# Kernel tuning notes

Hardware: AMD Instinct MI355X
Metric: run time of the kernel (lower is better)

Reference implementation:

```python
import jax, jax.numpy as jnp
import numpy as np

CDIM = 32
SCALES = (1, 16, 64, 256, 1024, 4096)  # last entry == T
INV_TEMP = 100.0
ENT_W = 0.1
COMMIT_W = 0.2
Q_SCALE = 1.0 / float(np.sqrt(CDIM))


def _interp_area(x, pt):
    # x: [B, T, C] -> [B, pt, C]; T divisible by pt so 'area' == block mean
    B, T, C = x.shape
    return x.reshape(B, pt, T // pt, C).mean(axis=2)


def _interp_linear(x, T):
    # x: [B, pt, C] -> [B, T, C]; mode='linear', align_corners=False
    pt = x.shape[1]
    pos = (jnp.arange(T, dtype=jnp.float32) + 0.5) * (pt / T) - 0.5
    pos = jnp.clip(pos, 0.0, pt - 1.0)
    lo = jnp.floor(pos).astype(jnp.int32)
    hi = jnp.minimum(lo + 1, pt - 1)
    w = (pos - lo.astype(jnp.float32))[None, :, None]
    return x[:, lo] * (1.0 - w) + x[:, hi] * w


def _bsq(f):
    # L2 normalize (torch F.normalize: clamp_min on norm)
    f = f / jnp.maximum(jnp.linalg.norm(f, axis=-1, keepdims=True), 1e-12)
    # sign quantize with STE
    zhat = jnp.where(f > 0, Q_SCALE, -Q_SCALE).astype(f.dtype)
    quantized = f + jax.lax.stop_gradient(zhat - f)
    # soft entropy loss
    p = jax.nn.sigmoid(-4.0 * f * (INV_TEMP / float(np.sqrt(CDIM))))
    prob = jnp.stack([p, 1.0 - p], axis=-1)  # [B, T, C, 2]
    ent = lambda c: -(c * jnp.log(c + 1e-8)).sum(axis=-1)
    per_sample_entropy = ent(prob).sum(axis=-1).mean()
    avg_prob = prob.mean(axis=(0, 1))  # [C, 2]
    cb_entropy = ent(avg_prob).sum()
    entropy_penalty = (per_sample_entropy - cb_entropy) / INV_TEMP
    commit = ((jax.lax.stop_gradient(quantized) - f) ** 2).sum(axis=-1).mean()
    aux = entropy_penalty * ENT_W + commit * COMMIT_W
    bits = (quantized > 0).astype(jnp.int32)
    return quantized, bits, aux


def setup_inputs() -> dict:
    key = jax.random.key(0)
    B, T, C = 128, SCALES[-1], CDIM
    return {"f_BTC": jax.random.normal(key, (B, T, C), dtype=jnp.float32)}


def reference(f_BTC):
    B, T, C = f_BTC.shape
    quantized_out = jnp.zeros_like(f_BTC)
    residual = f_BTC
    losses, bit_list = [], []
    for pt in SCALES:
        interp_res = _interp_area(residual, pt) if pt != T else residual
        q, bits, loss = _bsq(interp_res)
        q = _interp_linear(q, T) if pt != T else q
        residual = residual - jax.lax.stop_gradient(q)
        quantized_out = quantized_out + q
        bit_list.append(bits)
        losses.append(loss)
    all_losses = jnp.stack(losses, axis=-1)       # [num_scales]
    all_bits = jnp.concatenate(bit_list, axis=1)  # [B, sum(SCALES), C]
    return quantized_out, all_bits, all_losses
```

## Files before the change

kernel.cpp:

```cpp
#include <hip/hip_runtime.h>
#include <hip/hip_bf16.h>
#include <cstddef>
#include <cstdint>

#define NB 128
#define NT 4096
#define NC 32
#define BITROWS 5457
#define QV_ROWS 1361
#define QOUT_ELEMS (NB*NT*NC)
#define BITS_ELEMS (NB*BITROWS*NC)

#define ACC_OFF  22298624
#define S16_OFF  22302720

__device__ __constant__ float kQSC = 0.17677669529663687f;
__device__ __constant__ float kSIG = 17.67766952966369f;

__device__ __forceinline__ float interp_eval(const float* __restrict__ q, int P, int t, int c) {
  float pos = ((float)t + 0.5f) * ((float)P * (1.0f / 4096.0f)) - 0.5f;
  pos = fminf(fmaxf(pos, 0.0f), (float)(P - 1));
  const int lo = (int)pos;
  const int hi = min(lo + 1, P - 1);
  const float w = pos - (float)lo;
  const float a = __fmul_rn(q[lo * NC + c], 1.0f - w);
  const float b = __fmul_rn(q[hi * NC + c], w);
  return __fadd_rn(a, b);
}

__device__ __forceinline__ float interp_slice(const float* __restrict__ q, int P, int base, int t, int c) {
  float pos = ((float)t + 0.5f) * ((float)P * (1.0f / 4096.0f)) - 0.5f;
  pos = fminf(fmaxf(pos, 0.0f), (float)(P - 1));
  const int lo = (int)pos;
  const int hi = min(lo + 1, P - 1);
  const float w = pos - (float)lo;
  const float a = __fmul_rn(q[(lo - base) * NC + c], 1.0f - w);
  const float b = __fmul_rn(q[(hi - base) * NC + c], w);
  return __fadd_rn(a, b);
}

__device__ __forceinline__ void process_elem(
    float msum, float invn, int b, int rowOff, int j, int c,
    float* qlsRow, float* __restrict__ qvG, float* __restrict__ bitsG,
    float& entA, float& comA, float& pA)
{
  const float m = msum * invn;
  float ss = m * m;
  #pragma unroll
  for (int mk = 16; mk; mk >>= 1) ss += __shfl_xor(ss, mk, 32);
  const float den = fmaxf(sqrtf(ss), 1e-12f);
  const float fn = m / den;
  const bool bit = fn > 0.0f;
  const float zh = bit ? kQSC : -kQSC;
  const float qvv = fn + (zh - fn);
  if (qlsRow) qlsRow[c] = qvv;
  qvG[(size_t)b * (QV_ROWS * NC) + (size_t)(rowOff + j) * NC + c] = qvv;
  bitsG[(size_t)b * (BITROWS * NC) + (size_t)(rowOff + j) * NC + c] = bit ? 1.0f : 0.0f;
  const float arg = (-4.0f * fn) * kSIG;
  const float p = 1.0f / (1.0f + __expf(-arg));
  const float ent = -(p * __logf(p + 1e-8f) + (1.0f - p) * __logf((1.0f - p) + 1e-8f));
  const float d = qvv - fn;
  entA += ent; comA += d * d; pA += p;
}

__device__ __forceinline__ void reduce_losses(
    int sIdx, float entA, float comA, float pA, int tid, int nWaves,
    double* __restrict__ acc, float* redE, float* redC, float* redP)
{
  float e = entA, cm = comA;
  #pragma unroll
  for (int mk = 32; mk; mk >>= 1) { e += __shfl_xor(e, mk, 64); cm += __shfl_xor(cm, mk, 64); }
  const float p = pA + __shfl_xor(pA, 32, 64);
  const int w = tid >> 6, lane = tid & 63;
  if (lane == 0) { redE[w] = e; redC[w] = cm; }
  if (lane < 32) redP[w * 32 + lane] = p;
  __syncthreads();
  if (tid == 0) {
    double te = 0.0, tc = 0.0;
    for (int i = 0; i < nWaves; ++i) { te += (double)redE[i]; tc += (double)redC[i]; }
    atomicAdd(&acc[sIdx], te);
    atomicAdd(&acc[6 + sIdx], tc);
  }
  if (tid < 32) {
    float tp = 0.0f;
    for (int i = 0; i < nWaves; ++i) tp += redP[i * 32 + tid];
    atomicAdd(&acc[12 + sIdx * 32 + tid], (double)tp);
  }
  __syncthreads();
}

__global__ __launch_bounds__(256) void k_sum16(const float* __restrict__ f, float* __restrict__ S16) {
  const int idx = blockIdx.x * 256 + threadIdx.x;
  if (idx >= NB * 256 * NC) return;
  const int c = idx & 31;
  const int j = (idx >> 5) & 255;
  const int b = idx >> 13;
  const float* p = f + (size_t)b * (NT * NC) + (size_t)j * 16 * NC + c;
  float s = 0.0f;
  #pragma unroll
  for (int k = 0; k < 16; ++k) s += p[k * NC];
  S16[idx] = s;
}

__global__ __launch_bounds__(1024) void k_coarse(
    const float* __restrict__ S16g, float* __restrict__ qv,
    float* __restrict__ bitsOut, double* __restrict__ acc)
{
  __shared__ float S[256 * NC];
  __shared__ float qls[81 * NC];
  __shared__ float red[1024];
  __shared__ float redE[16], redC[16], redP[16 * 32];
  const int b = blockIdx.x, tid = threadIdx.x;
  const int c = tid & 31;

  for (int e = tid; e < 256 * NC; e += 1024) S[e] = S16g[(size_t)b * 8192 + e];
  __syncthreads();

  float entA, comA, pA;

  entA = comA = pA = 0.0f;
  {
    const int g = tid >> 5;
    float part = 0.0f;
    #pragma unroll
    for (int j = 0; j < 8; ++j) part += S[(g * 8 + j) * NC + c];
    red[tid] = part;
  }
  __syncthreads();
  if (tid < 32) {
    float msum = 0.0f;
    for (int g = 0; g < 32; ++g) msum += red[g * 32 + tid];
    process_elem(msum, 1.0f / 4096.0f, b, 0, 0, tid, &qls[0], qv, bitsOut, entA, comA, pA);
  }
  reduce_losses(0, entA, comA, pA, tid, 16, acc, redE, redC, redP);
  {
    const float corr = 16.0f * qls[c];
    for (int e = tid; e < 8192; e += 1024) S[e] -= corr;
  }
  __syncthreads();

  entA = comA = pA = 0.0f;
  if (tid < 512) {
    const int j = tid >> 5;
    float msum = 0.0f;
    for (int jj = 0; jj < 16; ++jj) msum += S[(j * 16 + jj) * NC + c];
    process_elem(msum, 1.0f / 256.0f, b, 1, j, c, &qls[(1 + j) * NC], qv, bitsOut, entA, comA, pA);
  }
  reduce_losses(1, entA, comA, pA, tid, 16, acc, redE, redC, redP);
  for (int e = tid; e < 8192; e += 1024) {
    const int jj = e >> 5;
    float cs = 0.0f;
    #pragma unroll
    for (int k = 0; k < 16; ++k) cs += interp_eval(&qls[1 * NC], 16, jj * 16 + k, c);
    S[e] -= cs;
  }
  __syncthreads();

  entA = comA = pA = 0.0f;
  for (int out = tid; out < 2048; out += 1024) {
    const int j = out >> 5;
    float msum = 0.0f;
    #pragma unroll
    for (int jj = 0; jj < 4; ++jj) msum += S[(j * 4 + jj) * NC + c];
    process_elem(msum, 1.0f / 64.0f, b, 17, j, c, &qls[(17 + j) * NC], qv, bitsOut, entA, comA, pA);
  }
  reduce_losses(2, entA, comA, pA, tid, 16, acc, redE, redC, redP);
  for (int e = tid; e < 8192; e += 1024) {
    const int jj = e >> 5;
    float cs = 0.0f;
    #pragma unroll
    for (int k = 0; k < 16; ++k) cs += interp_eval(&qls[17 * NC], 64, jj * 16 + k, c);
    S[e] -= cs;
  }
  __syncthreads();

  entA = comA = pA = 0.0f;
  for (int out = tid; out < 8192; out += 1024) {
    const int j = out >> 5;
    process_elem(S[out], 1.0f / 16.0f, b, 81, j, c, nullptr, qv, bitsOut, entA, comA, pA);
  }
  reduce_losses(3, entA, comA, pA, tid, 16, acc, redE, redC, redP);
}

__global__ __launch_bounds__(256) void k_scale4(
    const float* __restrict__ f, float* __restrict__ qv,
    float* __restrict__ bitsOut, double* __restrict__ acc)
{
  __shared__ float ql0[NC];
  __shared__ float ql1[3 * NC];
  __shared__ float ql2[6 * NC];
  __shared__ float ql3[18 * NC];
  __shared__ float redE[4], redC[4], redP[4 * 32];
  const int b = blockIdx.x >> 4, seg = blockIdx.x & 15;
  const int tid = threadIdx.x, c = tid & 31, rloc = tid >> 5;
  const float* __restrict__ qb = qv + (size_t)b * (QV_ROWS * NC);
  const int b1 = seg - 1, b2 = 4 * seg - 1, b3 = 16 * seg - 1;
  if (tid < NC) ql0[tid] = qb[tid];
  for (int e = tid; e < 3 * NC; e += 256) {
    const int r = min(max(b1 + (e >> 5), 0), 15);
    ql1[e] = qb[(1 + r) * NC + (e & 31)];
  }
  for (int e = tid; e < 6 * NC; e += 256) {
    const int r = min(max(b2 + (e >> 5), 0), 63);
    ql2[e] = qb[(17 + r) * NC + (e & 31)];
  }
  for (int e = tid; e < 18 * NC; e += 256) {
    const int r = min(max(b3 + (e >> 5), 0), 255);
    ql3[e] = qb[(81 + r) * NC + (e & 31)];
  }
  __syncthreads();
  float entA = 0.0f, comA = 0.0f, pA = 0.0f;
  for (int pass = 0; pass < 8; ++pass) {
    const int i = seg * 64 + pass * 8 + rloc;
    const float* fp = f + (size_t)b * (NT * NC) + (size_t)i * 4 * NC + c;
    float msum = 0.0f;
    #pragma unroll
    for (int k = 0; k < 4; ++k) {
      const int t = i * 4 + k;
      float r = fp[k * NC];
      r -= ql0[c];
      r -= interp_slice(ql1, 16,  b1, t, c);
      r -= interp_slice(ql2, 64,  b2, t, c);
      r -= interp_slice(ql3, 256, b3, t, c);
      msum += r;
    }
    process_elem(msum, 0.25f, b, 337, i, c, nullptr, qv, bitsOut, entA, comA, pA);
  }
  reduce_losses(4, entA, comA, pA, tid, 4, acc, redE, redC, redP);
}

__global__ __launch_bounds__(256) void k_final(
    const float* __restrict__ f, const float* __restrict__ qv,
    float* __restrict__ qout, float* __restrict__ bitsOut, double* __restrict__ acc)
{
  __shared__ float ql0[NC];
  __shared__ float ql1[3 * NC];
  __shared__ float ql2[6 * NC];
  __shared__ float ql3[18 * NC];
  __shared__ float ql4[66 * NC];
  __shared__ float redE[4], redC[4], redP[4 * 32];
  const int b = blockIdx.x >> 4, seg = blockIdx.x & 15;
  const int tid = threadIdx.x, c = tid & 31, rloc = tid >> 5;
  const int t0 = seg * 256;
  const float* __restrict__ qb = qv + (size_t)b * (QV_ROWS * NC);
  const int b1 = seg - 1, b2 = 4 * seg - 1, b3 = 16 * seg - 1, b4 = 64 * seg - 1;
  if (tid < NC) ql0[tid] = qb[tid];
  for (int e = tid; e < 3 * NC; e += 256) {
    const int r = min(max(b1 + (e >> 5), 0), 15);
    ql1[e] = qb[(1 + r) * NC + (e & 31)];
  }
  for (int e = tid; e < 6 * NC; e += 256) {
    const int r = min(max(b2 + (e >> 5), 0), 63);
    ql2[e] = qb[(17 + r) * NC + (e & 31)];
  }
  for (int e = tid; e < 18 * NC; e += 256) {
    const int r = min(max(b3 + (e >> 5), 0), 255);
    ql3[e] = qb[(81 + r) * NC + (e & 31)];
  }
  for (int e = tid; e < 66 * NC; e += 256) {
    const int r = min(max(b4 + (e >> 5), 0), 1023);
    ql4[e] = qb[(337 + r) * NC + (e & 31)];
  }
  __syncthreads();
  float entA = 0.0f, comA = 0.0f, pA = 0.0f;
  for (int pass = 0; pass < 32; ++pass) {
    const int t = t0 + pass * 8 + rloc;
    const float fv = f[(size_t)b * (NT * NC) + (size_t)t * NC + c];
    const float q0 = ql0[c];
    const float q1 = interp_slice(ql1, 16,   b1, t, c);
    const float q2 = interp_slice(ql2, 64,   b2, t, c);
    const float q3 = interp_slice(ql3, 256,  b3, t, c);
    const float q4 = interp_slice(ql4, 1024, b4, t, c);
    float r = fv;
    r -= q0; r -= q1; r -= q2; r -= q3; r -= q4;
    float qs = q0; qs += q1; qs += q2; qs += q3; qs += q4;
    float ss = r * r;
    #pragma unroll
    for (int mk = 16; mk; mk >>= 1) ss += __shfl_xor(ss, mk, 32);
    const float den = fmaxf(sqrtf(ss), 1e-12f);
    const float fn = r / den;
    const bool bit = fn > 0.0f;
    const float zh = bit ? kQSC : -kQSC;
    const float qvv = fn + (zh - fn);
    qout[(size_t)b * (NT * NC) + (size_t)t * NC + c] = qs + qvv;
    bitsOut[(size_t)b * (BITROWS * NC) + (size_t)(1361 + t) * NC + c] = bit ? 1.0f : 0.0f;
    const float arg = (-4.0f * fn) * kSIG;
    const float p = 1.0f / (1.0f + __expf(-arg));
    entA += -(p * __logf(p + 1e-8f) + (1.0f - p) * __logf((1.0f - p) + 1e-8f));
    const float d = qvv - fn;
    comA += d * d;
    pA += p;
  }
  reduce_losses(5, entA, comA, pA, tid, 4, acc, redE, redC, redP);
}

__global__ void k_losses(const double* __restrict__ acc, float* __restrict__ out) {
  const int s = threadIdx.x;
  if (s >= 6) return;
  const int pts[6] = {1, 16, 64, 256, 1024, 4096};
  const double n = 128.0 * (double)pts[s];
  const double pse = acc[s] / n;
  const double commit = acc[6 + s] / n;
  double cbe = 0.0;
  for (int c = 0; c < 32; ++c) {
    const double ap = acc[12 + s * 32 + c] / n;
    cbe += -(ap * log(ap + 1e-8) + (1.0 - ap) * log((1.0 - ap) + 1e-8));
  }
  const double pen = (pse - cbe) / 100.0;
  out[s] = (float)(pen * 0.1 + commit * 0.2);
}

extern "C" void kernel_launch(void* const* d_in, const int* in_sizes, int n_in,
                              void* d_out, int out_size, void* d_ws, size_t ws_size,
                              hipStream_t stream) {
  const float* f = (const float*)d_in[0];
  float* qout = (float*)d_out;
  float* bitsOut = qout + QOUT_ELEMS;
  float* lossesOut = qout + (QOUT_ELEMS + BITS_ELEMS);
  float* qv = (float*)d_ws;
  double* acc = (double*)((char*)d_ws + ACC_OFF);
  float* S16 = (float*)((char*)d_ws + S16_OFF);

  hipMemsetAsync(acc, 0, 204 * sizeof(double), stream);
  k_sum16<<<4096, 256, 0, stream>>>(f, S16);
  k_coarse<<<NB, 1024, 0, stream>>>(S16, qv, bitsOut, acc);
  k_scale4<<<NB * 16, 256, 0, stream>>>(f, qv, bitsOut, acc);
  k_final<<<NB * 16, 256, 0, stream>>>(f, qv, qout, bitsOut, acc);
  k_losses<<<1, 64, 0, stream>>>(acc, lossesOut);
}
```

Measured before the change: 354.5 us.

## Fuse scale-1024 stage into final kernel and fold 16-sum into coarse kernel

```diff
diff --git a/kernel.cpp b/kernel.cpp
--- a/kernel.cpp
+++ b/kernel.cpp
@@ -12,7 +12,6 @@
 #define BITS_ELEMS (NB*BITROWS*NC)
 
 #define ACC_OFF  22298624
-#define S16_OFF  22302720
 
 __device__ __constant__ float kQSC = 0.17677669529663687f;
 __device__ __constant__ float kSIG = 17.67766952966369f;
@@ -54,7 +53,7 @@
   const float zh = bit ? kQSC : -kQSC;
   const float qvv = fn + (zh - fn);
   if (qlsRow) qlsRow[c] = qvv;
-  qvG[(size_t)b * (QV_ROWS * NC) + (size_t)(rowOff + j) * NC + c] = qvv;
+  if (qvG) qvG[(size_t)b * (QV_ROWS * NC) + (size_t)(rowOff + j) * NC + c] = qvv;
   bitsG[(size_t)b * (BITROWS * NC) + (size_t)(rowOff + j) * NC + c] = bit ? 1.0f : 0.0f;
   const float arg = (-4.0f * fn) * kSIG;
   const float p = 1.0f / (1.0f + __expf(-arg));
@@ -89,21 +88,8 @@
   __syncthreads();
 }
 
-__global__ __launch_bounds__(256) void k_sum16(const float* __restrict__ f, float* __restrict__ S16) {
-  const int idx = blockIdx.x * 256 + threadIdx.x;
-  if (idx >= NB * 256 * NC) return;
-  const int c = idx & 31;
-  const int j = (idx >> 5) & 255;
-  const int b = idx >> 13;
-  const float* p = f + (size_t)b * (NT * NC) + (size_t)j * 16 * NC + c;
-  float s = 0.0f;
-  #pragma unroll
-  for (int k = 0; k < 16; ++k) s += p[k * NC];
-  S16[idx] = s;
-}
-
 __global__ __launch_bounds__(1024) void k_coarse(
-    const float* __restrict__ S16g, float* __restrict__ qv,
+    const float* __restrict__ f, float* __restrict__ qv,
     float* __restrict__ bitsOut, double* __restrict__ acc)
 {
   __shared__ float S[256 * NC];
@@ -113,7 +99,15 @@
   const int b = blockIdx.x, tid = threadIdx.x;
   const int c = tid & 31;
 
-  for (int e = tid; e < 256 * NC; e += 1024) S[e] = S16g[(size_t)b * 8192 + e];
+  for (int e = tid; e < 256 * NC; e += 1024) {
+    const int cc = e & 31;
+    const int j = e >> 5;
+    const float* p = f + (size_t)b * (NT * NC) + (size_t)j * 16 * NC + cc;
+    float s = 0.0f;
+    #pragma unroll
+    for (int k = 0; k < 16; ++k) s += p[k * NC];
+    S[e] = s;
+  }
   __syncthreads();
 
   float entA, comA, pA;
@@ -182,54 +176,7 @@
   reduce_losses(3, entA, comA, pA, tid, 16, acc, redE, redC, redP);
 }
 
-__global__ __launch_bounds__(256) void k_scale4(
-    const float* __restrict__ f, float* __restrict__ qv,
-    float* __restrict__ bitsOut, double* __restrict__ acc)
-{
-  __shared__ float ql0[NC];
-  __shared__ float ql1[3 * NC];
-  __shared__ float ql2[6 * NC];
-  __shared__ float ql3[18 * NC];
-  __shared__ float redE[4], redC[4], redP[4 * 32];
-  const int b = blockIdx.x >> 4, seg = blockIdx.x & 15;
-  const int tid = threadIdx.x, c = tid & 31, rloc = tid >> 5;
-  const float* __restrict__ qb = qv + (size_t)b * (QV_ROWS * NC);
-  const int b1 = seg - 1, b2 = 4 * seg - 1, b3 = 16 * seg - 1;
-  if (tid < NC) ql0[tid] = qb[tid];
-  for (int e = tid; e < 3 * NC; e += 256) {
-    const int r = min(max(b1 + (e >> 5), 0), 15);
-    ql1[e] = qb[(1 + r) * NC + (e & 31)];
-  }
-  for (int e = tid; e < 6 * NC; e += 256) {
-    const int r = min(max(b2 + (e >> 5), 0), 63);
-    ql2[e] = qb[(17 + r) * NC + (e & 31)];
-  }
-  for (int e = tid; e < 18 * NC; e += 256) {
-    const int r = min(max(b3 + (e >> 5), 0), 255);
-    ql3[e] = qb[(81 + r) * NC + (e & 31)];
-  }
-  __syncthreads();
-  float entA = 0.0f, comA = 0.0f, pA = 0.0f;
-  for (int pass = 0; pass < 8; ++pass) {
-    const int i = seg * 64 + pass * 8 + rloc;
-    const float* fp = f + (size_t)b * (NT * NC) + (size_t)i * 4 * NC + c;
-    float msum = 0.0f;
-    #pragma unroll
-    for (int k = 0; k < 4; ++k) {
-      const int t = i * 4 + k;
-      float r = fp[k * NC];
-      r -= ql0[c];
-      r -= interp_slice(ql1, 16,  b1, t, c);
-      r -= interp_slice(ql2, 64,  b2, t, c);
-      r -= interp_slice(ql3, 256, b3, t, c);
-      msum += r;
-    }
-    process_elem(msum, 0.25f, b, 337, i, c, nullptr, qv, bitsOut, entA, comA, pA);
-  }
-  reduce_losses(4, entA, comA, pA, tid, 4, acc, redE, redC, redP);
-}
-
-__global__ __launch_bounds__(256) void k_final(
+__global__ __launch_bounds__(256) void k_s45(
     const float* __restrict__ f, const float* __restrict__ qv,
     float* __restrict__ qout, float* __restrict__ bitsOut, double* __restrict__ acc)
 {
@@ -243,6 +190,7 @@
   const int tid = threadIdx.x, c = tid & 31, rloc = tid >> 5;
   const int t0 = seg * 256;
   const float* __restrict__ qb = qv + (size_t)b * (QV_ROWS * NC);
+  const float* __restrict__ fb = f + (size_t)b * (NT * NC);
   const int b1 = seg - 1, b2 = 4 * seg - 1, b3 = 16 * seg - 1, b4 = 64 * seg - 1;
   if (tid < NC) ql0[tid] = qb[tid];
   for (int e = tid; e < 3 * NC; e += 256) {
@@ -257,15 +205,59 @@
     const int r = min(max(b3 + (e >> 5), 0), 255);
     ql3[e] = qb[(81 + r) * NC + (e & 31)];
   }
-  for (int e = tid; e < 66 * NC; e += 256) {
-    const int r = min(max(b4 + (e >> 5), 0), 1023);
-    ql4[e] = qb[(337 + r) * NC + (e & 31)];
-  }
-  __syncthreads();
+  __syncthreads();
+
   float entA = 0.0f, comA = 0.0f, pA = 0.0f;
+  for (int pass = 0; pass < 8; ++pass) {
+    const int i = seg * 64 + pass * 8 + rloc;
+    const float* fp = fb + (size_t)i * 4 * NC + c;
+    float msum = 0.0f;
+    #pragma unroll
+    for (int k = 0; k < 4; ++k) {
+      const int t = i * 4 + k;
+      float r = fp[k * NC];
+      r -= ql0[c];
+      r -= interp_slice(ql1, 16,  b1, t, c);
+      r -= interp_slice(ql2, 64,  b2, t, c);
+      r -= interp_slice(ql3, 256, b3, t, c);
+      msum += r;
+    }
+    process_elem(msum, 0.25f, b, 337, i, c,
+                 &ql4[(size_t)(i - b4) * NC], nullptr, bitsOut, entA, comA, pA);
+  }
+  {
+    int hr = -1;
+    if (rloc == 0 && seg > 0)       hr = 64 * seg - 1;
+    else if (rloc == 1 && seg < 15) hr = 64 * seg + 64;
+    if (hr >= 0) {
+      const float* fp = fb + (size_t)hr * 4 * NC + c;
+      float msum = 0.0f;
+      #pragma unroll
+      for (int k = 0; k < 4; ++k) {
+        const int t = hr * 4 + k;
+        float r = fp[k * NC];
+        r -= ql0[c];
+        r -= interp_slice(ql1, 16,  b1, t, c);
+        r -= interp_slice(ql2, 64,  b2, t, c);
+        r -= interp_slice(ql3, 256, b3, t, c);
+        msum += r;
+      }
+      const float m = msum * 0.25f;
+      float ss = m * m;
+      #pragma unroll
+      for (int mk = 16; mk; mk >>= 1) ss += __shfl_xor(ss, mk, 32);
+      const float den = fmaxf(sqrtf(ss), 1e-12f);
+      const float fn = m / den;
+      const float zh = (fn > 0.0f) ? kQSC : -kQSC;
+      ql4[(size_t)(hr - b4) * NC + c] = fn + (zh - fn);
+    }
+  }
+  reduce_losses(4, entA, comA, pA, tid, 4, acc, redE, redC, redP);
+
+  entA = 0.0f; comA = 0.0f; pA = 0.0f;
   for (int pass = 0; pass < 32; ++pass) {
     const int t = t0 + pass * 8 + rloc;
-    const float fv = f[(size_t)b * (NT * NC) + (size_t)t * NC + c];
+    const float fv = fb[(size_t)t * NC + c];
     const float q0 = ql0[c];
     const float q1 = interp_slice(ql1, 16,   b1, t, c);
     const float q2 = interp_slice(ql2, 64,   b2, t, c);
@@ -319,12 +311,9 @@
   float* lossesOut = qout + (QOUT_ELEMS + BITS_ELEMS);
   float* qv = (float*)d_ws;
   double* acc = (double*)((char*)d_ws + ACC_OFF);
-  float* S16 = (float*)((char*)d_ws + S16_OFF);
 
   hipMemsetAsync(acc, 0, 204 * sizeof(double), stream);
-  k_sum16<<<4096, 256, 0, stream>>>(f, S16);
-  k_coarse<<<NB, 1024, 0, stream>>>(S16, qv, bitsOut, acc);
-  k_scale4<<<NB * 16, 256, 0, stream>>>(f, qv, bitsOut, acc);
-  k_final<<<NB * 16, 256, 0, stream>>>(f, qv, qout, bitsOut, acc);
+  k_coarse<<<NB, 1024, 0, stream>>>(f, qv, bitsOut, acc);
+  k_s45<<<NB * 16, 256, 0, stream>>>(f, qv, qout, bitsOut, acc);
   k_losses<<<1, 64, 0, stream>>>(acc, lossesOut);
 }
```

Result: faster. 335.0 us (-5.5%).
